# Optimization experiments

Measured on AMD Instinct MI355X. Metric: run time of the kernel, lower is better.

## Reference

```python
import jax, jax.numpy as jnp
import numpy as np

EMBED = 1024
HEADS = 16
B, T = 4, 2048


def setup_inputs() -> dict:
    key = jax.random.key(0)
    k1, k2, k3, k4, k5 = jax.random.split(key, 5)
    s_in = 1.0 / np.sqrt(EMBED)
    return {
        "x": jax.random.normal(k1, (B, T, EMBED), dtype=jnp.float32),
        "w_qkv": jax.random.uniform(k2, (3 * EMBED, EMBED), jnp.float32, -s_in, s_in),
        "b_qkv": jax.random.uniform(k3, (3 * EMBED,), jnp.float32, -s_in, s_in),
        "w_proj": jax.random.uniform(k4, (EMBED, EMBED), jnp.float32, -s_in, s_in),
        "b_proj": jax.random.uniform(k5, (EMBED,), jnp.float32, -s_in, s_in),
    }


def reference(x, w_qkv, b_qkv, w_proj, b_proj):
    Bz, Tz, C = x.shape
    nh = HEADS
    hs = C // nh
    qkv = jnp.einsum('btc,oc->bto', x, w_qkv) + b_qkv  # [B,T,3C]
    q, k, v = jnp.split(qkv, 3, axis=-1)
    # [B, nh, T, hs]
    q = q.reshape(Bz, Tz, nh, hs).transpose(0, 2, 1, 3)
    k = k.reshape(Bz, Tz, nh, hs).transpose(0, 2, 1, 3)
    v = v.reshape(Bz, Tz, nh, hs).transpose(0, 2, 1, 3)
    scale = 1.0 / np.sqrt(hs).astype(np.float32)
    att = jnp.einsum('bhqd,bhkd->bhqk', q, k) * scale
    causal_mask = jnp.tril(jnp.ones((Tz, Tz), dtype=bool))
    att = jnp.where(causal_mask[None, None], att, jnp.finfo(att.dtype).min)
    att = jax.nn.softmax(att, axis=-1)
    y = jnp.einsum('bhqk,bhkd->bhqd', att, v)
    y = y.transpose(0, 2, 1, 3).reshape(Bz, Tz, C)
    return jnp.einsum('btc,oc->bto', y, w_proj) + b_proj
```

## Files before the change

kernel.cpp:

```cpp
#include <hip/hip_runtime.h>

typedef __bf16 bf16x8 __attribute__((ext_vector_type(8)));
typedef float f32x4 __attribute__((ext_vector_type(4)));

#define DI __device__ __forceinline__

#define WAIT_VMCNT(N)                                        \
  do {                                                       \
    __builtin_amdgcn_sched_barrier(0);                       \
    asm volatile("s_waitcnt vmcnt(" #N ")" ::: "memory");    \
    __builtin_amdgcn_sched_barrier(0);                       \
  } while (0)

DI unsigned short f2bf(float f) {
  unsigned int u = __float_as_uint(f);
  u += 0x7FFFu + ((u >> 16) & 1u);
  return (unsigned short)(u >> 16);
}

DI unsigned cvt_pk_bf16(float a, float b) {
  unsigned r;
  asm("v_cvt_pk_bf16_f32 %0, %1, %2" : "=v"(r) : "v"(a), "v"(b));
  return r;
}

DI float exp2_fast(float x) {
  float r;
  asm("v_exp_f32 %0, %1" : "=v"(r) : "v"(x));
  return r;
}

DI void fence() { asm volatile("" ::: "memory"); }
DI void bar() { fence(); __builtin_amdgcn_s_barrier(); fence(); }

DI bf16x8 ld16(const void* p) {
  union { uint4 u; bf16x8 b; } c;
  c.u = *reinterpret_cast<const uint4*>(p);
  return c.b;
}

DI f32x4 mfma16(bf16x8 a, bf16x8 b, f32x4 c) {
  return __builtin_amdgcn_mfma_f32_16x16x32_bf16(a, b, c, 0, 0, 0);
}

DI void gload_lds16(const void* g, void* l) {
  __builtin_amdgcn_global_load_lds(
      (const __attribute__((address_space(1))) unsigned int*)g,
      (__attribute__((address_space(3))) unsigned int*)l, 16, 0, 0);
}

__global__ void cvt_all(const float* __restrict__ x, const float* __restrict__ wq,
                        const float* __restrict__ wp,
                        unsigned short* __restrict__ xb, unsigned short* __restrict__ wqb,
                        unsigned short* __restrict__ wpb) {
  int i = blockIdx.x * blockDim.x + threadIdx.x;
  const float* s;
  unsigned short* d;
  int off;
  if (i < 2097152) { s = x; d = xb; off = i; }
  else if (i < 2097152 + 786432) { s = wq; d = wqb; off = i - 2097152; }
  else { s = wp; d = wpb; off = i - (2097152 + 786432); }
  float4 v = reinterpret_cast<const float4*>(s)[off];
  uint2 o;
  o.x = cvt_pk_bf16(v.x, v.y);
  o.y = cvt_pk_bf16(v.z, v.w);
  reinterpret_cast<uint2*>(d)[off] = o;
}

template <int N, int MODE>
__global__ __launch_bounds__(256)
void gemm_bt(const unsigned short* __restrict__ A,
             const unsigned short* __restrict__ W,
             const float* __restrict__ bias,
             float* __restrict__ out,
             unsigned short* __restrict__ qo,
             unsigned short* __restrict__ ko,
             unsigned short* __restrict__ vo) {
  constexpr int K = 1024;
  __shared__ __align__(16) char smem[32768];
  char* Asm = smem;
  char* Bsm = smem + 16384;
  const int tid = threadIdx.x;
  const int ln = tid & 63;
  const int w  = tid >> 6;
  const int wm = w >> 1, wn = w & 1;
  const int g = ln >> 4, q = ln & 15;
  const int m0 = blockIdx.x * 128;
  const int n0 = blockIdx.y * 128;

  f32x4 acc[4][4] = {};

  for (int kt = 0; kt < K / 64; ++kt) {
    if (kt) bar();
#pragma unroll
    for (int i = 0; i < 4; ++i) {
      const int chunk = i * 4 + w;
      const int o = chunk * 1024 + ln * 16;
      const int row = o >> 7;
      const int colb = (o & 127) ^ ((row & 7) << 4);
      gload_lds16((const char*)A + ((size_t)(m0 + row) * K + kt * 64) * 2 + colb,
                  Asm + chunk * 1024);
      gload_lds16((const char*)W + ((size_t)(n0 + row) * K + kt * 64) * 2 + colb,
                  Bsm + chunk * 1024);
    }
    WAIT_VMCNT(0);
    bar();
#pragma unroll
    for (int ks = 0; ks < 2; ++ks) {
      bf16x8 av[4], bv[4];
#pragma unroll
      for (int mf = 0; mf < 4; ++mf) {
        const int row = wm * 64 + mf * 16 + q;
        av[mf] = ld16(Asm + ((row * 128 + ks * 64 + g * 16) ^ ((row & 7) << 4)));
      }
#pragma unroll
      for (int nf = 0; nf < 4; ++nf) {
        const int row = wn * 64 + nf * 16 + q;
        bv[nf] = ld16(Bsm + ((row * 128 + ks * 64 + g * 16) ^ ((row & 7) << 4)));
      }
#pragma unroll
      for (int mf = 0; mf < 4; ++mf)
#pragma unroll
        for (int nf = 0; nf < 4; ++nf)
          acc[mf][nf] = mfma16(av[mf], bv[nf], acc[mf][nf]);
    }
  }

#pragma unroll
  for (int nf = 0; nf < 4; ++nf) {
    const int col = n0 + wn * 64 + nf * 16 + q;
    const float bv = bias[col];
#pragma unroll
    for (int mf = 0; mf < 4; ++mf) {
      const int rbase = m0 + wm * 64 + mf * 16 + g * 4;
#pragma unroll
      for (int r = 0; r < 4; ++r) {
        const int row = rbase + r;
        const float v = acc[mf][nf][r] + bv;
        if constexpr (MODE == 0) {
          out[(size_t)row * N + col] = v;
        } else {
          const int b = row >> 11, t = row & 2047;
          if (col < 1024) {
            const int h = col >> 6, d = col & 63;
            qo[((((size_t)b * 16 + h) << 11) + t) * 64 + d] = f2bf(v * 0.18033688011112042f);
          } else if (col < 2048) {
            const int c = col - 1024;
            const int h = c >> 6, d = c & 63;
            ko[((((size_t)b * 16 + h) << 11) + t) * 64 + d] = f2bf(v);
          } else {
            const int c = col - 2048;
            const int h = c >> 6, d = c & 63;
            vo[((((size_t)b * 16 + h) << 6) + d) * 2048 + t] = f2bf(v);
          }
        }
      }
    }
  }
}

__global__ __launch_bounds__(256)
void attn_fwd(const unsigned short* __restrict__ Qb,
              const unsigned short* __restrict__ Kb,
              const unsigned short* __restrict__ Vtb,
              unsigned short* __restrict__ Yb) {
  __shared__ __align__(16) char smem[49152];
  char* Psm = smem + 32768;
  const int tid = threadIdx.x;
  const int ln = tid & 63;
  const int w = tid >> 6;
  const int g = ln >> 4, q = ln & 15;
  const int qt = 15 - blockIdx.y;
  const int bh = blockIdx.x;
  const int q0 = qt * 128;
  const int qw = q0 + w * 32;
  const size_t base = (size_t)bh * 2048 * 64;

  bf16x8 qf[2][2];
#pragma unroll
  for (int nf = 0; nf < 2; ++nf)
#pragma unroll
    for (int kf = 0; kf < 2; ++kf)
      qf[nf][kf] = ld16(Qb + base + (size_t)(qw + nf * 16 + q) * 64 + kf * 32 + g * 8);
  WAIT_VMCNT(0);

  float m_run[2] = {-INFINITY, -INFINITY};
  float l_run[2] = {0.f, 0.f};
  f32x4 yt[4][2] = {};

  auto stage = [&](int j, int buf) {
    char* Kd = smem + buf * 16384;
    char* Vd = Kd + 8192;
    const int kv0 = j << 6;
    const char* Kg = (const char*)(Kb + base + (size_t)kv0 * 64);
    const char* Vg = (const char*)(Vtb + base) + kv0 * 2;
#pragma unroll
    for (int i = 0; i < 2; ++i) {
      const int chunk = i * 4 + w;
      const int o = chunk * 1024 + ln * 16;
      const int row = o >> 7;
      const int colb = (o & 127) ^ ((row & 7) << 4);
      gload_lds16(Kg + row * 128 + colb, Kd + chunk * 1024);
      gload_lds16(Vg + (size_t)row * 4096 + colb, Vd + chunk * 1024);
    }
  };

  const int nkv = (q0 >> 6) + 2;
  stage(0, 0);
  for (int j = 0; j < nkv; ++j) {
    if (j + 1 < nkv) {
      stage(j + 1, (j + 1) & 1);
      WAIT_VMCNT(4);
    } else {
      WAIT_VMCNT(0);
    }
    bar();

    const int kv0 = j << 6;
    const char* Ksm = smem + (j & 1) * 16384;
    const char* Vsm = Ksm + 8192;
    const bool active = (kv0 <= qw + 31);
    if (active) {
      f32x4 st[4][2] = {};
      __builtin_amdgcn_s_setprio(1);
#pragma unroll
      for (int mf = 0; mf < 4; ++mf) {
        const int row = mf * 16 + q;
        const int swz = (row & 7) << 4;
        const bf16x8 a0 = ld16(Ksm + ((row * 128 + g * 16) ^ swz));
        const bf16x8 a1 = ld16(Ksm + ((row * 128 + 64 + g * 16) ^ swz));
#pragma unroll
        for (int nf = 0; nf < 2; ++nf) {
          st[mf][nf] = mfma16(a0, qf[nf][0], st[mf][nf]);
          st[mf][nf] = mfma16(a1, qf[nf][1], st[mf][nf]);
        }
      }
      __builtin_amdgcn_s_setprio(0);
      if (kv0 + 63 > qw) {
#pragma unroll
        for (int mf = 0; mf < 4; ++mf)
#pragma unroll
          for (int nf = 0; nf < 2; ++nf)
#pragma unroll
            for (int r = 0; r < 4; ++r)
              if (kv0 + mf * 16 + g * 4 + r > qw + nf * 16 + q)
                st[mf][nf][r] = -INFINITY;
      }
#pragma unroll
      for (int nf = 0; nf < 2; ++nf) {
        float vmax = -INFINITY;
#pragma unroll
        for (int mf = 0; mf < 4; ++mf) {
          const f32x4 v = st[mf][nf];
          vmax = fmaxf(fmaxf(vmax, fmaxf(v[0], v[1])), fmaxf(v[2], v[3]));
        }
        vmax = fmaxf(vmax, __shfl_xor(vmax, 16));
        vmax = fmaxf(vmax, __shfl_xor(vmax, 32));
        const float mo = m_run[nf];
        if (__any(vmax > mo)) {
          const float mn = fmaxf(mo, vmax);
          const float corr = exp2_fast(mo - mn);
          m_run[nf] = mn;
          l_run[nf] *= corr;
#pragma unroll
          for (int mfd = 0; mfd < 4; ++mfd) yt[mfd][nf] *= corr;
        }
        const float mcur = m_run[nf];
        float ls = 0.f;
#pragma unroll
        for (int mf = 0; mf < 4; ++mf) {
          f32x4 p;
#pragma unroll
          for (int r = 0; r < 4; ++r) p[r] = exp2_fast(st[mf][nf][r] - mcur);
          ls += (p[0] + p[1]) + (p[2] + p[3]);
          uint2 pk2;
          pk2.x = cvt_pk_bf16(p[0], p[1]);
          pk2.y = cvt_pk_bf16(p[2], p[3]);
          const int prow = w * 32 + nf * 16 + q;
          *(uint2*)(Psm + ((prow * 128 + mf * 32 + g * 8) ^ ((prow & 7) << 4))) = pk2;
        }
        ls += __shfl_xor(ls, 16);
        ls += __shfl_xor(ls, 32);
        l_run[nf] += ls;
      }
      __builtin_amdgcn_s_setprio(1);
#pragma unroll
      for (int kf = 0; kf < 2; ++kf) {
        bf16x8 pb[2];
#pragma unroll
        for (int nf = 0; nf < 2; ++nf) {
          const int prow = w * 32 + nf * 16 + q;
          pb[nf] = ld16(Psm + ((prow * 128 + kf * 64 + g * 16) ^ ((prow & 7) << 4)));
        }
#pragma unroll
        for (int mfd = 0; mfd < 4; ++mfd) {
          const int vrow = mfd * 16 + q;
          const bf16x8 vv = ld16(Vsm + ((vrow * 128 + kf * 64 + g * 16) ^ ((vrow & 7) << 4)));
#pragma unroll
          for (int nf = 0; nf < 2; ++nf)
            yt[mfd][nf] = mfma16(vv, pb[nf], yt[mfd][nf]);
        }
      }
      __builtin_amdgcn_s_setprio(0);
    }
    bar();
  }

  const int b = bh >> 4, h = bh & 15;
#pragma unroll
  for (int nf = 0; nf < 2; ++nf) {
    const float inv = 1.f / l_run[nf];
    const int qr = qw + nf * 16 + q;
    unsigned short* yp = Yb + (size_t)(b * 2048 + qr) * 1024 + h * 64;
#pragma unroll
    for (int mfd = 0; mfd < 4; ++mfd) {
      uint2 o2;
      o2.x = cvt_pk_bf16(yt[mfd][nf][0] * inv, yt[mfd][nf][1] * inv);
      o2.y = cvt_pk_bf16(yt[mfd][nf][2] * inv, yt[mfd][nf][3] * inv);
      *(uint2*)(yp + mfd * 16 + g * 4) = o2;
    }
  }
}

extern "C" void kernel_launch(void* const* d_in, const int* in_sizes, int n_in,
                              void* d_out, int out_size, void* d_ws, size_t ws_size,
                              hipStream_t stream) {
  const float* x      = (const float*)d_in[0];
  const float* w_qkv  = (const float*)d_in[1];
  const float* b_qkv  = (const float*)d_in[2];
  const float* w_proj = (const float*)d_in[3];
  const float* b_proj = (const float*)d_in[4];
  float* out = (float*)d_out;
  char* ws = (char*)d_ws;

  unsigned short* xb  = (unsigned short*)(ws);
  unsigned short* wqb = (unsigned short*)(ws + (size_t)(16 << 20));
  unsigned short* wpb = (unsigned short*)(ws + (size_t)(22 << 20));
  unsigned short* Qb  = (unsigned short*)(ws + (size_t)(24 << 20));
  unsigned short* Kb  = (unsigned short*)(ws + (size_t)(40 << 20));
  unsigned short* Vtb = (unsigned short*)(ws + (size_t)(56 << 20));
  unsigned short* Yb  = (unsigned short*)(ws + (size_t)(72 << 20));

  cvt_all<<<12288, 256, 0, stream>>>(x, w_qkv, w_proj, xb, wqb, wpb);
  gemm_bt<3072, 1><<<dim3(64, 24), 256, 0, stream>>>(xb, wqb, b_qkv, nullptr, Qb, Kb, Vtb);
  attn_fwd<<<dim3(64, 16), 256, 0, stream>>>(Qb, Kb, Vtb, Yb);
  gemm_bt<1024, 0><<<dim3(64, 8), 256, 0, stream>>>(Yb, wpb, b_proj, out, nullptr, nullptr, nullptr);
}
```

Before: 189.1 us.

## Pair causal query tiles per attention block and vectorize transposed V stores

Each attention block now handles two query tiles (15-p and p), so every block does the same amount of causal work. The grid shrinks from 1024 to 512 blocks. This targets the load imbalance and tail from triangular work, at the cost of fewer blocks and less latency hiding. Separately, the QKV GEMM epilogue now packs four consecutive t values of transposed V into one 8-byte store instead of four scalar stores, and hoists the Q/K address math out of the per-row loop.

```diff
diff --git a/kernel.cpp b/kernel.cpp
--- a/kernel.cpp
+++ b/kernel.cpp
@@ -133,26 +133,32 @@
 #pragma unroll
     for (int mf = 0; mf < 4; ++mf) {
       const int rbase = m0 + wm * 64 + mf * 16 + g * 4;
-#pragma unroll
-      for (int r = 0; r < 4; ++r) {
-        const int row = rbase + r;
-        const float v = acc[mf][nf][r] + bv;
-        if constexpr (MODE == 0) {
-          out[(size_t)row * N + col] = v;
+      if constexpr (MODE == 0) {
+#pragma unroll
+        for (int r = 0; r < 4; ++r)
+          out[(size_t)(rbase + r) * N + col] = acc[mf][nf][r] + bv;
+      } else {
+        const int b = rbase >> 11, t0 = rbase & 2047;
+        if (col < 1024) {
+          const int h = col >> 6, d = col & 63;
+          unsigned short* qp = qo + ((((size_t)b * 16 + h) << 11) + t0) * 64 + d;
+#pragma unroll
+          for (int r = 0; r < 4; ++r)
+            qp[r * 64] = f2bf((acc[mf][nf][r] + bv) * 0.18033688011112042f);
+        } else if (col < 2048) {
+          const int c = col - 1024;
+          const int h = c >> 6, d = c & 63;
+          unsigned short* kp = ko + ((((size_t)b * 16 + h) << 11) + t0) * 64 + d;
+#pragma unroll
+          for (int r = 0; r < 4; ++r)
+            kp[r * 64] = f2bf(acc[mf][nf][r] + bv);
         } else {
-          const int b = row >> 11, t = row & 2047;
-          if (col < 1024) {
-            const int h = col >> 6, d = col & 63;
-            qo[((((size_t)b * 16 + h) << 11) + t) * 64 + d] = f2bf(v * 0.18033688011112042f);
-          } else if (col < 2048) {
-            const int c = col - 1024;
-            const int h = c >> 6, d = c & 63;
-            ko[((((size_t)b * 16 + h) << 11) + t) * 64 + d] = f2bf(v);
-          } else {
-            const int c = col - 2048;
-            const int h = c >> 6, d = c & 63;
-            vo[((((size_t)b * 16 + h) << 6) + d) * 2048 + t] = f2bf(v);
-          }
+          const int c = col - 2048;
+          const int h = c >> 6, d = c & 63;
+          uint2 pk;
+          pk.x = cvt_pk_bf16(acc[mf][nf][0] + bv, acc[mf][nf][1] + bv);
+          pk.y = cvt_pk_bf16(acc[mf][nf][2] + bv, acc[mf][nf][3] + bv);
+          *(uint2*)(vo + ((((size_t)b * 16 + h) << 6) + d) * 2048 + t0) = pk;
         }
       }
     }
@@ -170,23 +176,10 @@
   const int ln = tid & 63;
   const int w = tid >> 6;
   const int g = ln >> 4, q = ln & 15;
-  const int qt = 15 - blockIdx.y;
   const int bh = blockIdx.x;
-  const int q0 = qt * 128;
-  const int qw = q0 + w * 32;
+  const int pair = blockIdx.y;
   const size_t base = (size_t)bh * 2048 * 64;
-
-  bf16x8 qf[2][2];
-#pragma unroll
-  for (int nf = 0; nf < 2; ++nf)
-#pragma unroll
-    for (int kf = 0; kf < 2; ++kf)
-      qf[nf][kf] = ld16(Qb + base + (size_t)(qw + nf * 16 + q) * 64 + kf * 32 + g * 8);
-  WAIT_VMCNT(0);
-
-  float m_run[2] = {-INFINITY, -INFINITY};
-  float l_run[2] = {0.f, 0.f};
-  f32x4 yt[4][2] = {};
+  const int b = bh >> 4, h = bh & 15;
 
   auto stage = [&](int j, int buf) {
     char* Kd = smem + buf * 16384;
@@ -205,121 +198,140 @@
     }
   };
 
-  const int nkv = (q0 >> 6) + 2;
-  stage(0, 0);
-  for (int j = 0; j < nkv; ++j) {
-    if (j + 1 < nkv) {
-      stage(j + 1, (j + 1) & 1);
-      WAIT_VMCNT(4);
-    } else {
-      WAIT_VMCNT(0);
-    }
-    bar();
-
-    const int kv0 = j << 6;
-    const char* Ksm = smem + (j & 1) * 16384;
-    const char* Vsm = Ksm + 8192;
-    const bool active = (kv0 <= qw + 31);
-    if (active) {
-      f32x4 st[4][2] = {};
-      __builtin_amdgcn_s_setprio(1);
-#pragma unroll
-      for (int mf = 0; mf < 4; ++mf) {
-        const int row = mf * 16 + q;
-        const int swz = (row & 7) << 4;
-        const bf16x8 a0 = ld16(Ksm + ((row * 128 + g * 16) ^ swz));
-        const bf16x8 a1 = ld16(Ksm + ((row * 128 + 64 + g * 16) ^ swz));
+  auto run_qtile = [&](int qt) {
+    const int q0 = qt * 128;
+    const int qw = q0 + w * 32;
+
+    bf16x8 qf[2][2];
+#pragma unroll
+    for (int nf = 0; nf < 2; ++nf)
+#pragma unroll
+      for (int kf = 0; kf < 2; ++kf)
+        qf[nf][kf] = ld16(Qb + base + (size_t)(qw + nf * 16 + q) * 64 + kf * 32 + g * 8);
+    WAIT_VMCNT(0);
+
+    float m_run[2] = {-INFINITY, -INFINITY};
+    float l_run[2] = {0.f, 0.f};
+    f32x4 yt[4][2] = {};
+
+    const int nkv = (q0 >> 6) + 2;
+    stage(0, 0);
+    for (int j = 0; j < nkv; ++j) {
+      if (j + 1 < nkv) {
+        stage(j + 1, (j + 1) & 1);
+        WAIT_VMCNT(4);
+      } else {
+        WAIT_VMCNT(0);
+      }
+      bar();
+
+      const int kv0 = j << 6;
+      const char* Ksm = smem + (j & 1) * 16384;
+      const char* Vsm = Ksm + 8192;
+      const bool active = (kv0 <= qw + 31);
+      if (active) {
+        f32x4 st[4][2] = {};
+        __builtin_amdgcn_s_setprio(1);
+#pragma unroll
+        for (int mf = 0; mf < 4; ++mf) {
+          const int row = mf * 16 + q;
+          const int swz = (row & 7) << 4;
+          const bf16x8 a0 = ld16(Ksm + ((row * 128 + g * 16) ^ swz));
+          const bf16x8 a1 = ld16(Ksm + ((row * 128 + 64 + g * 16) ^ swz));
+#pragma unroll
+          for (int nf = 0; nf < 2; ++nf) {
+            st[mf][nf] = mfma16(a0, qf[nf][0], st[mf][nf]);
+            st[mf][nf] = mfma16(a1, qf[nf][1], st[mf][nf]);
+          }
+        }
+        __builtin_amdgcn_s_setprio(0);
+        if (kv0 + 63 > qw) {
+#pragma unroll
+          for (int mf = 0; mf < 4; ++mf)
+#pragma unroll
+            for (int nf = 0; nf < 2; ++nf)
+#pragma unroll
+              for (int r = 0; r < 4; ++r)
+                if (kv0 + mf * 16 + g * 4 + r > qw + nf * 16 + q)
+                  st[mf][nf][r] = -INFINITY;
+        }
 #pragma unroll
         for (int nf = 0; nf < 2; ++nf) {
-          st[mf][nf] = mfma16(a0, qf[nf][0], st[mf][nf]);
-          st[mf][nf] = mfma16(a1, qf[nf][1], st[mf][nf]);
-        }
-      }
-      __builtin_amdgcn_s_setprio(0);
-      if (kv0 + 63 > qw) {
-#pragma unroll
-        for (int mf = 0; mf < 4; ++mf)
-#pragma unroll
-          for (int nf = 0; nf < 2; ++nf)
-#pragma unroll
-            for (int r = 0; r < 4; ++r)
-              if (kv0 + mf * 16 + g * 4 + r > qw + nf * 16 + q)
-                st[mf][nf][r] = -INFINITY;
-      }
-#pragma unroll
-      for (int nf = 0; nf < 2; ++nf) {
-        float vmax = -INFINITY;
-#pragma unroll
-        for (int mf = 0; mf < 4; ++mf) {
-          const f32x4 v = st[mf][nf];
-          vmax = fmaxf(fmaxf(vmax, fmaxf(v[0], v[1])), fmaxf(v[2], v[3]));
-        }
-        vmax = fmaxf(vmax, __shfl_xor(vmax, 16));
-        vmax = fmaxf(vmax, __shfl_xor(vmax, 32));
-        const float mo = m_run[nf];
-        if (__any(vmax > mo)) {
-          const float mn = fmaxf(mo, vmax);
-          const float corr = exp2_fast(mo - mn);
-          m_run[nf] = mn;
-          l_run[nf] *= corr;
-#pragma unroll
-          for (int mfd = 0; mfd < 4; ++mfd) yt[mfd][nf] *= corr;
-        }
-        const float mcur = m_run[nf];
-        float ls = 0.f;
-#pragma unroll
-        for (int mf = 0; mf < 4; ++mf) {
-          f32x4 p;
-#pragma unroll
-          for (int r = 0; r < 4; ++r) p[r] = exp2_fast(st[mf][nf][r] - mcur);
-          ls += (p[0] + p[1]) + (p[2] + p[3]);
-          uint2 pk2;
-          pk2.x = cvt_pk_bf16(p[0], p[1]);
-          pk2.y = cvt_pk_bf16(p[2], p[3]);
-          const int prow = w * 32 + nf * 16 + q;
-          *(uint2*)(Psm + ((prow * 128 + mf * 32 + g * 8) ^ ((prow & 7) << 4))) = pk2;
-        }
-        ls += __shfl_xor(ls, 16);
-        ls += __shfl_xor(ls, 32);
-        l_run[nf] += ls;
-      }
-      __builtin_amdgcn_s_setprio(1);
-#pragma unroll
-      for (int kf = 0; kf < 2; ++kf) {
-        bf16x8 pb[2];
-#pragma unroll
-        for (int nf = 0; nf < 2; ++nf) {
-          const int prow = w * 32 + nf * 16 + q;
-          pb[nf] = ld16(Psm + ((prow * 128 + kf * 64 + g * 16) ^ ((prow & 7) << 4)));
-        }
-#pragma unroll
-        for (int mfd = 0; mfd < 4; ++mfd) {
-          const int vrow = mfd * 16 + q;
-          const bf16x8 vv = ld16(Vsm + ((vrow * 128 + kf * 64 + g * 16) ^ ((vrow & 7) << 4)));
-#pragma unroll
-          for (int nf = 0; nf < 2; ++nf)
-            yt[mfd][nf] = mfma16(vv, pb[nf], yt[mfd][nf]);
-        }
-      }
-      __builtin_amdgcn_s_setprio(0);
-    }
-    bar();
-  }
-
-  const int b = bh >> 4, h = bh & 15;
-#pragma unroll
-  for (int nf = 0; nf < 2; ++nf) {
-    const float inv = 1.f / l_run[nf];
-    const int qr = qw + nf * 16 + q;
-    unsigned short* yp = Yb + (size_t)(b * 2048 + qr) * 1024 + h * 64;
-#pragma unroll
-    for (int mfd = 0; mfd < 4; ++mfd) {
-      uint2 o2;
-      o2.x = cvt_pk_bf16(yt[mfd][nf][0] * inv, yt[mfd][nf][1] * inv);
-      o2.y = cvt_pk_bf16(yt[mfd][nf][2] * inv, yt[mfd][nf][3] * inv);
-      *(uint2*)(yp + mfd * 16 + g * 4) = o2;
-    }
-  }
+          float vmax = -INFINITY;
+#pragma unroll
+          for (int mf = 0; mf < 4; ++mf) {
+            const f32x4 v = st[mf][nf];
+            vmax = fmaxf(fmaxf(vmax, fmaxf(v[0], v[1])), fmaxf(v[2], v[3]));
+          }
+          vmax = fmaxf(vmax, __shfl_xor(vmax, 16));
+          vmax = fmaxf(vmax, __shfl_xor(vmax, 32));
+          const float mo = m_run[nf];
+          if (__any(vmax > mo)) {
+            const float mn = fmaxf(mo, vmax);
+            const float corr = exp2_fast(mo - mn);
+            m_run[nf] = mn;
+            l_run[nf] *= corr;
+#pragma unroll
+            for (int mfd = 0; mfd < 4; ++mfd) yt[mfd][nf] *= corr;
+          }
+          const float mcur = m_run[nf];
+          float ls = 0.f;
+#pragma unroll
+          for (int mf = 0; mf < 4; ++mf) {
+            f32x4 p;
+#pragma unroll
+            for (int r = 0; r < 4; ++r) p[r] = exp2_fast(st[mf][nf][r] - mcur);
+            ls += (p[0] + p[1]) + (p[2] + p[3]);
+            uint2 pk2;
+            pk2.x = cvt_pk_bf16(p[0], p[1]);
+            pk2.y = cvt_pk_bf16(p[2], p[3]);
+            const int prow = w * 32 + nf * 16 + q;
+            *(uint2*)(Psm + ((prow * 128 + mf * 32 + g * 8) ^ ((prow & 7) << 4))) = pk2;
+          }
+          ls += __shfl_xor(ls, 16);
+          ls += __shfl_xor(ls, 32);
+          l_run[nf] += ls;
+        }
+        __builtin_amdgcn_s_setprio(1);
+#pragma unroll
+        for (int kf = 0; kf < 2; ++kf) {
+          bf16x8 pb[2];
+#pragma unroll
+          for (int nf = 0; nf < 2; ++nf) {
+            const int prow = w * 32 + nf * 16 + q;
+            pb[nf] = ld16(Psm + ((prow * 128 + kf * 64 + g * 16) ^ ((prow & 7) << 4)));
+          }
+#pragma unroll
+          for (int mfd = 0; mfd < 4; ++mfd) {
+            const int vrow = mfd * 16 + q;
+            const bf16x8 vv = ld16(Vsm + ((vrow * 128 + kf * 64 + g * 16) ^ ((vrow & 7) << 4)));
+#pragma unroll
+            for (int nf = 0; nf < 2; ++nf)
+              yt[mfd][nf] = mfma16(vv, pb[nf], yt[mfd][nf]);
+          }
+        }
+        __builtin_amdgcn_s_setprio(0);
+      }
+      bar();
+    }
+
+#pragma unroll
+    for (int nf = 0; nf < 2; ++nf) {
+      const float inv = 1.f / l_run[nf];
+      const int qr = qw + nf * 16 + q;
+      unsigned short* yp = Yb + (size_t)(b * 2048 + qr) * 1024 + h * 64;
+#pragma unroll
+      for (int mfd = 0; mfd < 4; ++mfd) {
+        uint2 o2;
+        o2.x = cvt_pk_bf16(yt[mfd][nf][0] * inv, yt[mfd][nf][1] * inv);
+        o2.y = cvt_pk_bf16(yt[mfd][nf][2] * inv, yt[mfd][nf][3] * inv);
+        *(uint2*)(yp + mfd * 16 + g * 4) = o2;
+      }
+    }
+  };
+
+  run_qtile(15 - pair);
+  run_qtile(pair);
 }
 
 extern "C" void kernel_launch(void* const* d_in, const int* in_sizes, int n_in,
@@ -343,6 +355,6 @@
 
   cvt_all<<<12288, 256, 0, stream>>>(x, w_qkv, w_proj, xb, wqb, wpb);
   gemm_bt<3072, 1><<<dim3(64, 24), 256, 0, stream>>>(xb, wqb, b_qkv, nullptr, Qb, Kb, Vtb);
-  attn_fwd<<<dim3(64, 16), 256, 0, stream>>>(Qb, Kb, Vtb, Yb);
+  attn_fwd<<<dim3(64, 8), 256, 0, stream>>>(Qb, Kb, Vtb, Yb);
   gemm_bt<1024, 0><<<dim3(64, 8), 256, 0, stream>>>(Yb, wpb, b_proj, out, nullptr, nullptr, nullptr);
 }
```

Result: faster. 174.2 us (-7.9%).
